# Kernel optimization log

Hardware: AMD Instinct MI355X
Metric: run time of the kernel (lower is better)

Reference implementation:

```python
import jax, jax.numpy as jnp
import numpy as np


def setup_inputs() -> dict:
    key = jax.random.key(0)
    k1, k2, k3, k4 = jax.random.split(key, 4)
    T, H, E, I = 4096, 1024, 8, 3584
    return {
        "hidden_states": jax.random.normal(k1, (T, H), dtype=jnp.float32),
        "gate_w": jax.random.normal(k2, (H, E), dtype=jnp.float32) * 0.02,
        "w1": jax.random.normal(k3, (E, H, I), dtype=jnp.float32) * 0.02,
        "w2": jax.random.normal(k4, (E, I, H), dtype=jnp.float32) * 0.02,
        "top_k": 2,
    }


def reference(hidden_states, gate_w, w1, w2, top_k):
    # Router: logits -> softmax -> top-k -> renormalize (Mixtral / vLLM fused_moe)
    router_logits = hidden_states @ gate_w                    # [T, E]
    probs = jax.nn.softmax(router_logits, axis=-1)
    top_vals, top_idx = jax.lax.top_k(probs, top_k)           # [T, K]
    top_vals = top_vals / jnp.sum(top_vals, axis=-1, keepdims=True)
    E = gate_w.shape[1]
    # Dense per-(token, expert) combine weights, zero for non-selected experts
    dense_w = jnp.sum(jax.nn.one_hot(top_idx, E, dtype=hidden_states.dtype)
                      * top_vals[..., None], axis=1)          # [T, E]
    # Expert MLP: silu(x @ w1[e]) @ w2[e], weighted by routing probs
    act = jax.nn.silu(jnp.einsum('th,ehi->tei', hidden_states, w1))  # [T, E, I]
    act = act * dense_w[:, :, None]
    out = jnp.einsum('tei,eih->th', act, w2)                  # [T, H]
    return out
```

## Files before the change

### kernel.cpp

```cpp
#include <hip/hip_runtime.h>
#include <hip/hip_bf16.h>

#define T_TOK 4096
#define H_DIM 1024
#define E_NUM 8
#define I_DIM 3584
#define NPAIR (T_TOK * 2)
#define MAX_RT 72

#define BM 128
#define BN 128
#define BK 64

typedef __attribute__((ext_vector_type(8))) short bf16x8;
typedef __attribute__((ext_vector_type(4))) float f32x4;
typedef __attribute__((ext_vector_type(8))) unsigned short ushort8_t;
typedef __attribute__((ext_vector_type(4))) unsigned short ushort4_t;

__device__ __forceinline__ unsigned short f2bf(float x) {
  unsigned int u = __float_as_uint(x);
  unsigned int r = (u + 0x7FFFu + ((u >> 16) & 1u)) >> 16;
  return (unsigned short)r;
}

__device__ __forceinline__ void gload16(const void* g, unsigned short* l) {
  __builtin_amdgcn_global_load_lds(
      (const __attribute__((address_space(1))) void*)g,
      (__attribute__((address_space(3))) void*)l, 16, 0, 0);
}

__global__ void transpose_cvt(const float* __restrict__ src,
                              unsigned short* __restrict__ dst, int R, int C) {
  __shared__ float tile[64][65];
  const int e = blockIdx.z;
  const int c0 = blockIdx.x * 64, r0 = blockIdx.y * 64;
  const float* s = src + (size_t)e * R * C;
  unsigned short* d = dst + (size_t)e * R * C;
  const int th = threadIdx.x;
  const int tr = th >> 4;
  const int tc4 = (th & 15) * 4;
#pragma unroll
  for (int it = 0; it < 4; ++it) {
    const int r = it * 16 + tr;
    float4 v = *reinterpret_cast<const float4*>(s + (size_t)(r0 + r) * C + c0 + tc4);
    tile[r][tc4] = v.x; tile[r][tc4 + 1] = v.y; tile[r][tc4 + 2] = v.z; tile[r][tc4 + 3] = v.w;
  }
  __syncthreads();
  const int wc = th >> 3;
  const int wr = (th & 7) * 8;
#pragma unroll
  for (int it = 0; it < 2; ++it) {
    const int c = it * 32 + wc;
    ushort8_t o;
#pragma unroll
    for (int j = 0; j < 8; ++j) o[j] = f2bf(tile[wr + j][c]);
    *reinterpret_cast<ushort8_t*>(d + (size_t)(c0 + c) * R + r0 + wr) = o;
  }
}

__global__ void router_kernel(const float* __restrict__ hs, const float* __restrict__ gw,
                              unsigned short* __restrict__ hsb,
                              int* __restrict__ eid, float* __restrict__ wgt,
                              int* __restrict__ counts) {
  __shared__ float s_gw[8192];
  __shared__ int s_cnt[E_NUM];
  const int th = threadIdx.x;
  for (int u = th; u < 2048; u += 256) {
    const f32x4 v = *reinterpret_cast<const f32x4*>(gw + u * 4);
    *reinterpret_cast<f32x4*>(&s_gw[(u ^ ((u >> 3) & 7)) * 4]) = v;
  }
  if (th < E_NUM) s_cnt[th] = 0;
  __syncthreads();

  const int l = th & 63, w = th >> 6;
#pragma unroll 1
  for (int tt = 0; tt < 4; ++tt) {
    const int t = blockIdx.x * 16 + w * 4 + tt;
    const float* hrow = hs + (size_t)t * H_DIM;
    unsigned short* brow = hsb + (size_t)t * H_DIM;
    float acc[E_NUM];
#pragma unroll
    for (int e = 0; e < E_NUM; ++e) acc[e] = 0.f;
#pragma unroll
    for (int i = 0; i < 4; ++i) {
      const int h0 = i * 256 + l * 4;
      const f32x4 x = *reinterpret_cast<const f32x4*>(hrow + h0);
      ushort4_t o = { f2bf(x[0]), f2bf(x[1]), f2bf(x[2]), f2bf(x[3]) };
      *reinterpret_cast<ushort4_t*>(brow + h0) = o;
#pragma unroll
      for (int j = 0; j < 4; ++j) {
        const int h = h0 + j;
        const int p0 = (h * 2) ^ ((h >> 2) & 7);
        const f32x4 g0 = *reinterpret_cast<const f32x4*>(&s_gw[p0 * 4]);
        const f32x4 g1 = *reinterpret_cast<const f32x4*>(&s_gw[(p0 ^ 1) * 4]);
        acc[0] += x[j] * g0[0]; acc[1] += x[j] * g0[1];
        acc[2] += x[j] * g0[2]; acc[3] += x[j] * g0[3];
        acc[4] += x[j] * g1[0]; acc[5] += x[j] * g1[1];
        acc[6] += x[j] * g1[2]; acc[7] += x[j] * g1[3];
      }
    }
#pragma unroll
    for (int e = 0; e < E_NUM; ++e) {
#pragma unroll
      for (int off = 1; off < 64; off <<= 1) acc[e] += __shfl_xor(acc[e], off);
    }
    if (l == 0) {
      int i1 = 0;
#pragma unroll
      for (int e = 1; e < E_NUM; ++e) if (acc[e] > acc[i1]) i1 = e;
      int i2 = (i1 == 0) ? 1 : 0;
#pragma unroll
      for (int e = 0; e < E_NUM; ++e) if (e != i1 && acc[e] > acc[i2]) i2 = e;
      const float e2 = __expf(acc[i2] - acc[i1]);
      const float inv = 1.f / (1.f + e2);
      eid[t * 2] = i1;     wgt[t * 2] = inv;
      eid[t * 2 + 1] = i2; wgt[t * 2 + 1] = e2 * inv;
      atomicAdd(&s_cnt[i1], 1);
      atomicAdd(&s_cnt[i2], 1);
    }
  }
  __syncthreads();
  if (th < E_NUM && s_cnt[th] > 0) atomicAdd(&counts[th], s_cnt[th]);
}

__global__ void scatter_kernel(const int* __restrict__ eid, const int* __restrict__ counts,
                               int* __restrict__ fill, int* __restrict__ rowmap) {
  __shared__ int hist[E_NUM], base[E_NUM];
  const int th = threadIdx.x;
  const int p = blockIdx.x * 256 + th;
  if (th < E_NUM) hist[th] = 0;
  __syncthreads();
  const int e = eid[p];
  const int rloc = atomicAdd(&hist[e], 1);
  __syncthreads();
  if (th < E_NUM) base[th] = (hist[th] > 0) ? atomicAdd(&fill[th], hist[th]) : 0;
  __syncthreads();
  int off = 0;
#pragma unroll
  for (int i = 0; i < E_NUM; ++i) off += (i < e) ? counts[i] : 0;
  rowmap[off + base[e] + rloc] = p;
}

template <int MODE, int NCT>
__launch_bounds__(256, 3)
__global__ void moe_gemm(const unsigned short* __restrict__ hsb,
                         const unsigned short* __restrict__ wt,
                         const unsigned short* __restrict__ act_in,
                         unsigned short* __restrict__ act_out,
                         float* __restrict__ out,
                         const int* __restrict__ counts,
                         const int* __restrict__ rowmap,
                         const float* __restrict__ wgt) {
  constexpr int KD = (MODE == 0) ? H_DIM : I_DIM;
  constexpr int NWG = MAX_RT * NCT;

  __shared__ unsigned short As[BM * BK];
  __shared__ unsigned short Bs[BN * BK];
  __shared__ int s_pair[BM];
  __shared__ float s_w[BM];

  const int bid = blockIdx.x;
  const int wgid = (bid & 7) * (NWG / 8) + (bid >> 3);
  const int rt = wgid / NCT;
  const int ct = wgid % NCT;

  int e = -1, loc_rt = 0, off_e = 0, cnt = 0;
  {
    int acc_t = 0, off = 0;
#pragma unroll
    for (int ee = 0; ee < E_NUM; ++ee) {
      const int c = counts[ee];
      const int nt = (c + BM - 1) >> 7;
      if (e < 0 && rt < acc_t + nt) { e = ee; loc_rt = rt - acc_t; off_e = off; cnt = c; }
      acc_t += nt; off += c;
    }
  }
  if (e < 0) return;

  const int cnt_local = min(BM, cnt - loc_rt * BM);
  const int r_base = off_e + loc_rt * BM;
  const int th = threadIdx.x;
  const int lane = th & 63, wid = th >> 6;

  if (MODE == 1 && th < BM) {
    int r = loc_rt * BM + th;
    if (r >= cnt) r = cnt - 1;
    const int p = rowmap[off_e + r];
    s_pair[th] = p;
    s_w[th] = wgt[p];
  }

  const int n0 = ct * BN;
  const unsigned short* wbase = wt + (size_t)e * ((size_t)I_DIM * H_DIM) + (size_t)n0 * KD;

  const int srow = lane >> 3;
  const int cg = (lane & 7) ^ srow;
  const char* aptr[4];
  const char* bptr[4];
#pragma unroll
  for (int i = 0; i < 4; ++i) {
    const int r = i * 32 + wid * 8 + srow;
    const int rr = (r < cnt_local) ? r : (cnt_local - 1);
    if (MODE == 0) {
      const int tok = rowmap[off_e + loc_rt * BM + rr] >> 1;
      aptr[i] = (const char*)(hsb + (size_t)tok * H_DIM) + cg * 16;
    } else {
      aptr[i] = (const char*)(act_in + (size_t)(r_base + rr) * I_DIM) + cg * 16;
    }
    bptr[i] = (const char*)(wbase + (size_t)r * KD) + cg * 16;
  }
  unsigned short* dstA[4];
  unsigned short* dstB[4];
#pragma unroll
  for (int i = 0; i < 4; ++i) {
    dstA[i] = &As[(i * 32 + wid * 8) * BK];
    dstB[i] = &Bs[(i * 32 + wid * 8) * BK];
  }

  f32x4 acc[4][4];
#pragma unroll
  for (int m = 0; m < 4; ++m)
#pragma unroll
    for (int n = 0; n < 4; ++n) acc[m][n] = (f32x4){0.f, 0.f, 0.f, 0.f};

  const int wm = (wid >> 1) * 64;
  const int wn = (wid & 1) * 64;
  const int fr = lane & 15;
  const int fq = lane >> 4;
  const int sxor = fr & 7;

  for (int k0 = 0; k0 < KD; k0 += BK) {
    const int kb = k0 * 2;
#pragma unroll
    for (int i = 0; i < 4; ++i) gload16(aptr[i] + kb, dstA[i]);
#pragma unroll
    for (int i = 0; i < 4; ++i) gload16(bptr[i] + kb, dstB[i]);
    __syncthreads();

#pragma unroll
    for (int kk = 0; kk < 2; ++kk) {
      bf16x8 af[4], bf[4];
#pragma unroll
      for (int m = 0; m < 4; ++m)
        af[m] = *reinterpret_cast<const bf16x8*>(
            &As[(wm + m * 16 + fr) * BK + ((kk * 4 + fq) ^ sxor) * 8]);
#pragma unroll
      for (int n = 0; n < 4; ++n)
        bf[n] = *reinterpret_cast<const bf16x8*>(
            &Bs[(wn + n * 16 + fr) * BK + ((kk * 4 + fq) ^ sxor) * 8]);
#pragma unroll
      for (int m = 0; m < 4; ++m)
#pragma unroll
        for (int n = 0; n < 4; ++n)
          acc[m][n] = __builtin_amdgcn_mfma_f32_16x16x32_bf16(af[m], bf[n], acc[m][n], 0, 0, 0);
    }
    __syncthreads();
  }

#pragma unroll
  for (int m = 0; m < 4; ++m) {
    const int row = wm + m * 16 + fq * 4;
#pragma unroll
    for (int n = 0; n < 4; ++n) {
      const int col = wn + n * 16 + fr;
#pragma unroll
      for (int r = 0; r < 4; ++r) {
        const int rw = row + r;
        if (rw < cnt_local) {
          const float x = acc[m][n][r];
          if (MODE == 0) {
            const float s = x / (1.f + __expf(-x));
            act_out[(size_t)(r_base + rw) * I_DIM + n0 + col] = f2bf(s);
          } else {
            const int p = s_pair[rw];
            const int tok = p >> 1;
            atomicAdd(out + (size_t)tok * H_DIM + n0 + col, x * s_w[rw]);
          }
        }
      }
    }
  }
}

extern "C" void kernel_launch(void* const* d_in, const int* in_sizes, int n_in,
                              void* d_out, int out_size, void* d_ws, size_t ws_size,
                              hipStream_t stream) {
  const float* hs = (const float*)d_in[0];
  const float* gw = (const float*)d_in[1];
  const float* w1 = (const float*)d_in[2];
  const float* w2 = (const float*)d_in[3];
  float* out = (float*)d_out;

  char* ws = (char*)d_ws;
  const size_t WMAT = (size_t)E_NUM * I_DIM * H_DIM * 2;
  unsigned short* w1t = (unsigned short*)ws;
  unsigned short* w2t = (unsigned short*)(ws + WMAT);
  unsigned short* act = (unsigned short*)(ws + 2 * WMAT);
  unsigned short* hsb = (unsigned short*)(ws + 3 * WMAT);
  char* small = ws + 3 * WMAT + (size_t)T_TOK * H_DIM * 2;
  int* eid = (int*)small;
  float* wgt = (float*)(small + NPAIR * 4);
  int* rowmap = (int*)(small + 2 * NPAIR * 4);
  int* counts = (int*)(small + 3 * NPAIR * 4);
  int* fill = counts + 8;

  hipMemsetAsync(d_out, 0, (size_t)T_TOK * H_DIM * sizeof(float), stream);
  hipMemsetAsync(counts, 0, 16 * sizeof(int), stream);

  transpose_cvt<<<dim3(I_DIM / 64, H_DIM / 64, E_NUM), 256, 0, stream>>>(w1, w1t, H_DIM, I_DIM);
  transpose_cvt<<<dim3(H_DIM / 64, I_DIM / 64, E_NUM), 256, 0, stream>>>(w2, w2t, I_DIM, H_DIM);

  router_kernel<<<T_TOK / 16, 256, 0, stream>>>(hs, gw, hsb, eid, wgt, counts);
  scatter_kernel<<<NPAIR / 256, 256, 0, stream>>>(eid, counts, fill, rowmap);

  moe_gemm<0, I_DIM / BN><<<MAX_RT * (I_DIM / BN), 256, 0, stream>>>(
      hsb, w1t, nullptr, act, nullptr, counts, rowmap, wgt);
  moe_gemm<1, H_DIM / BN><<<MAX_RT * (H_DIM / BN), 256, 0, stream>>>(
      hsb, w2t, act, nullptr, out, counts, rowmap, wgt);
}
```

Measured before the change: 286.4 us.

## Pipeline MoE GEMM with triple-buffered LDS ring, 256-wide tiles and split-K down-projection

Reworks the expert GEMM into a 512-thread workgroup with 128x256 tiles and a three-stage LDS ring buffer. Global-to-LDS loads for later K steps are issued while MFMAs run on the current stage, with explicit waitcnt, barriers and setprio. The second GEMM is split along K into four chunks that accumulate through the existing atomics, which restores parallelism after widening N. This raises LDS use and occupancy pressure and adds more atomic traffic on the output.

```diff
diff --git a/kernel.cpp b/kernel.cpp
--- a/kernel.cpp
+++ b/kernel.cpp
@@ -9,7 +9,7 @@
 #define MAX_RT 72
 
 #define BM 128
-#define BN 128
+#define BN 256
 #define BK 64
 
 typedef __attribute__((ext_vector_type(8))) short bf16x8;
@@ -141,8 +141,8 @@
   rowmap[off + base[e] + rloc] = p;
 }
 
-template <int MODE, int NCT>
-__launch_bounds__(256, 3)
+template <int MODE, int NCT, int KS, int KBLK>
+__launch_bounds__(512, 2)
 __global__ void moe_gemm(const unsigned short* __restrict__ hsb,
                          const unsigned short* __restrict__ wt,
                          const unsigned short* __restrict__ act_in,
@@ -151,18 +151,21 @@
                          const int* __restrict__ counts,
                          const int* __restrict__ rowmap,
                          const float* __restrict__ wgt) {
-  constexpr int KD = (MODE == 0) ? H_DIM : I_DIM;
-  constexpr int NWG = MAX_RT * NCT;
-
-  __shared__ unsigned short As[BM * BK];
-  __shared__ unsigned short Bs[BN * BK];
+  constexpr int KROW = (MODE == 0) ? H_DIM : I_DIM;
+  constexpr int NT = KBLK / BK;
+  constexpr int NWG = MAX_RT * NCT * KS;
+  constexpr int RING = 24576;
+
+  __shared__ unsigned short S[3 * RING];
   __shared__ int s_pair[BM];
   __shared__ float s_w[BM];
 
   const int bid = blockIdx.x;
   const int wgid = (bid & 7) * (NWG / 8) + (bid >> 3);
-  const int rt = wgid / NCT;
-  const int ct = wgid % NCT;
+  const int rt = wgid / (NCT * KS);
+  const int rem = wgid % (NCT * KS);
+  const int ct = rem % NCT;
+  const int kbase = (rem / NCT) * KBLK;
 
   int e = -1, loc_rt = 0, off_e = 0, cnt = 0;
   {
@@ -191,31 +194,47 @@
   }
 
   const int n0 = ct * BN;
-  const unsigned short* wbase = wt + (size_t)e * ((size_t)I_DIM * H_DIM) + (size_t)n0 * KD;
-
-  const int srow = lane >> 3;
-  const int cg = (lane & 7) ^ srow;
-  const char* aptr[4];
+  const unsigned short* wbase =
+      wt + (size_t)e * ((size_t)I_DIM * H_DIM) + (size_t)n0 * KROW + kbase;
+
+  const int srow8 = lane >> 3;
+  const int cg = (lane & 7) ^ srow8;
+  const char* aptr[2];
   const char* bptr[4];
 #pragma unroll
-  for (int i = 0; i < 4; ++i) {
-    const int r = i * 32 + wid * 8 + srow;
+  for (int i = 0; i < 2; ++i) {
+    const int r = i * 64 + wid * 8 + srow8;
     const int rr = (r < cnt_local) ? r : (cnt_local - 1);
     if (MODE == 0) {
       const int tok = rowmap[off_e + loc_rt * BM + rr] >> 1;
-      aptr[i] = (const char*)(hsb + (size_t)tok * H_DIM) + cg * 16;
+      aptr[i] = (const char*)(hsb + (size_t)tok * H_DIM + kbase) + cg * 16;
     } else {
-      aptr[i] = (const char*)(act_in + (size_t)(r_base + rr) * I_DIM) + cg * 16;
-    }
-    bptr[i] = (const char*)(wbase + (size_t)r * KD) + cg * 16;
-  }
-  unsigned short* dstA[4];
-  unsigned short* dstB[4];
-#pragma unroll
-  for (int i = 0; i < 4; ++i) {
-    dstA[i] = &As[(i * 32 + wid * 8) * BK];
-    dstB[i] = &Bs[(i * 32 + wid * 8) * BK];
-  }
+      aptr[i] = (const char*)(act_in + (size_t)(r_base + rr) * I_DIM + kbase) + cg * 16;
+    }
+  }
+#pragma unroll
+  for (int j = 0; j < 4; ++j) {
+    const int r = j * 64 + wid * 8 + srow8;
+    bptr[j] = (const char*)(wbase + (size_t)r * KROW) + cg * 16;
+  }
+
+#define STG_P0(rg, kb) do {                                     \
+    gload16(aptr[0] + (kb), &S[(rg) * RING + wid * 512]);       \
+    gload16(aptr[1] + (kb), &S[(rg) * RING + 4096 + wid * 512]);\
+    gload16(bptr[0] + (kb), &S[(rg) * RING + 8192 + wid * 512]);} while (0)
+#define STG_P1(rg, kb) do {                                     \
+    gload16(bptr[1] + (kb), &S[(rg) * RING + 12288 + wid * 512]);\
+    gload16(bptr[2] + (kb), &S[(rg) * RING + 16384 + wid * 512]);\
+    gload16(bptr[3] + (kb), &S[(rg) * RING + 20480 + wid * 512]);} while (0)
+
+  const int wm = (wid >> 2) * 64;
+  const int wn = (wid & 3) * 64;
+  const int fr = lane & 15, fq = lane >> 4;
+  const int sx = fr & 7;
+  const int ck0 = (fq ^ sx) * 8;
+  const int ck1 = ((4 + fq) ^ sx) * 8;
+  const int arow = (wm + fr) * 64;
+  const int brow = (wn + fr) * 64;
 
   f32x4 acc[4][4];
 #pragma unroll
@@ -223,58 +242,87 @@
 #pragma unroll
     for (int n = 0; n < 4; ++n) acc[m][n] = (f32x4){0.f, 0.f, 0.f, 0.f};
 
-  const int wm = (wid >> 1) * 64;
-  const int wn = (wid & 1) * 64;
-  const int fr = lane & 15;
-  const int fq = lane >> 4;
-  const int sxor = fr & 7;
-
-  for (int k0 = 0; k0 < KD; k0 += BK) {
-    const int kb = k0 * 2;
-#pragma unroll
-    for (int i = 0; i < 4; ++i) gload16(aptr[i] + kb, dstA[i]);
-#pragma unroll
-    for (int i = 0; i < 4; ++i) gload16(bptr[i] + kb, dstB[i]);
-    __syncthreads();
-
-#pragma unroll
-    for (int kk = 0; kk < 2; ++kk) {
-      bf16x8 af[4], bf[4];
+  STG_P0(0, 0); STG_P1(0, 0);
+  STG_P0(1, 128); STG_P1(1, 128);
+  asm volatile("s_waitcnt vmcnt(6)" ::: "memory");
+  __builtin_amdgcn_s_barrier();
+
+  int rd = 0, wr = 2;
+  for (int t = 0; t < NT; ++t) {
+    const unsigned short* Ab = &S[rd * RING];
+    const unsigned short* Bb = Ab + 8192;
+    const int kb2 = (t + 2) * 128;
+    const bool stg = (t + 2) < NT;
+    {
+      bf16x8 a0[4], b0[4];
 #pragma unroll
       for (int m = 0; m < 4; ++m)
-        af[m] = *reinterpret_cast<const bf16x8*>(
-            &As[(wm + m * 16 + fr) * BK + ((kk * 4 + fq) ^ sxor) * 8]);
+        a0[m] = *reinterpret_cast<const bf16x8*>(&Ab[arow + m * 1024 + ck0]);
 #pragma unroll
       for (int n = 0; n < 4; ++n)
-        bf[n] = *reinterpret_cast<const bf16x8*>(
-            &Bs[(wn + n * 16 + fr) * BK + ((kk * 4 + fq) ^ sxor) * 8]);
+        b0[n] = *reinterpret_cast<const bf16x8*>(&Bb[brow + n * 1024 + ck0]);
+      if (stg) STG_P0(wr, kb2);
+      __builtin_amdgcn_s_barrier();
+      asm volatile("s_waitcnt lgkmcnt(0)" ::: "memory");
+      __builtin_amdgcn_sched_barrier(0);
+      __builtin_amdgcn_s_setprio(1);
 #pragma unroll
       for (int m = 0; m < 4; ++m)
 #pragma unroll
         for (int n = 0; n < 4; ++n)
-          acc[m][n] = __builtin_amdgcn_mfma_f32_16x16x32_bf16(af[m], bf[n], acc[m][n], 0, 0, 0);
-    }
-    __syncthreads();
-  }
+          acc[m][n] = __builtin_amdgcn_mfma_f32_16x16x32_bf16(a0[m], b0[n], acc[m][n], 0, 0, 0);
+      __builtin_amdgcn_s_setprio(0);
+      __builtin_amdgcn_s_barrier();
+    }
+    {
+      bf16x8 a1[4], b1[4];
+#pragma unroll
+      for (int m = 0; m < 4; ++m)
+        a1[m] = *reinterpret_cast<const bf16x8*>(&Ab[arow + m * 1024 + ck1]);
+#pragma unroll
+      for (int n = 0; n < 4; ++n)
+        b1[n] = *reinterpret_cast<const bf16x8*>(&Bb[brow + n * 1024 + ck1]);
+      if (stg) STG_P1(wr, kb2);
+      __builtin_amdgcn_s_barrier();
+      asm volatile("s_waitcnt lgkmcnt(0)" ::: "memory");
+      __builtin_amdgcn_sched_barrier(0);
+      __builtin_amdgcn_s_setprio(1);
+#pragma unroll
+      for (int m = 0; m < 4; ++m)
+#pragma unroll
+        for (int n = 0; n < 4; ++n)
+          acc[m][n] = __builtin_amdgcn_mfma_f32_16x16x32_bf16(a1[m], b1[n], acc[m][n], 0, 0, 0);
+      __builtin_amdgcn_s_setprio(0);
+    }
+    if (t + 1 < NT) {
+      if (stg) asm volatile("s_waitcnt vmcnt(6)" ::: "memory");
+      else     asm volatile("s_waitcnt vmcnt(0)" ::: "memory");
+      __builtin_amdgcn_sched_barrier(0);
+      __builtin_amdgcn_s_barrier();
+    }
+    rd = (rd == 2) ? 0 : rd + 1;
+    wr = (wr == 2) ? 0 : wr + 1;
+  }
+#undef STG_P0
+#undef STG_P1
 
 #pragma unroll
   for (int m = 0; m < 4; ++m) {
     const int row = wm + m * 16 + fq * 4;
 #pragma unroll
     for (int n = 0; n < 4; ++n) {
-      const int col = wn + n * 16 + fr;
-#pragma unroll
-      for (int r = 0; r < 4; ++r) {
-        const int rw = row + r;
+      const int col = n0 + wn + n * 16 + fr;
+#pragma unroll
+      for (int r2 = 0; r2 < 4; ++r2) {
+        const int rw = row + r2;
         if (rw < cnt_local) {
-          const float x = acc[m][n][r];
+          const float x = acc[m][n][r2];
           if (MODE == 0) {
             const float s = x / (1.f + __expf(-x));
-            act_out[(size_t)(r_base + rw) * I_DIM + n0 + col] = f2bf(s);
+            act_out[(size_t)(r_base + rw) * I_DIM + col] = f2bf(s);
           } else {
-            const int p = s_pair[rw];
-            const int tok = p >> 1;
-            atomicAdd(out + (size_t)tok * H_DIM + n0 + col, x * s_w[rw]);
+            const int tok = s_pair[rw] >> 1;
+            atomicAdd(out + (size_t)tok * H_DIM + col, x * s_w[rw]);
           }
         }
       }
@@ -313,8 +361,8 @@
   router_kernel<<<T_TOK / 16, 256, 0, stream>>>(hs, gw, hsb, eid, wgt, counts);
   scatter_kernel<<<NPAIR / 256, 256, 0, stream>>>(eid, counts, fill, rowmap);
 
-  moe_gemm<0, I_DIM / BN><<<MAX_RT * (I_DIM / BN), 256, 0, stream>>>(
+  moe_gemm<0, 14, 1, 1024><<<MAX_RT * 14, 512, 0, stream>>>(
       hsb, w1t, nullptr, act, nullptr, counts, rowmap, wgt);
-  moe_gemm<1, H_DIM / BN><<<MAX_RT * (H_DIM / BN), 256, 0, stream>>>(
+  moe_gemm<1, 4, 4, 896><<<MAX_RT * 4 * 4, 512, 0, stream>>>(
       hsb, w2t, act, nullptr, out, counts, rowmap, wgt);
 }
```

Result: slower. 371.4 us (+29.7%).

## Double-buffer LDS tiles to overlap global loads with MFMA compute

Applied to the files above, without the earlier changes.

Converts the MoE GEMM main loop to a two-stage LDS ping-pong: the next K-tile is prefetched directly into the alternate buffer while the current tile's fragments are read and fed to MFMAs, with one barrier per iteration instead of two. It also hoists all fragment loads ahead of the MFMA block and raises wave priority during the math. Doubling LDS means occupancy drops from 3 to 2 blocks per CU (launch bounds changed accordingly), which trades latency hiding by occupancy for explicit software pipelining.

```diff
diff --git a/kernel.cpp b/kernel.cpp
--- a/kernel.cpp
+++ b/kernel.cpp
@@ -142,7 +142,7 @@
 }
 
 template <int MODE, int NCT>
-__launch_bounds__(256, 3)
+__launch_bounds__(256, 2)
 __global__ void moe_gemm(const unsigned short* __restrict__ hsb,
                          const unsigned short* __restrict__ wt,
                          const unsigned short* __restrict__ act_in,
@@ -152,10 +152,11 @@
                          const int* __restrict__ rowmap,
                          const float* __restrict__ wgt) {
   constexpr int KD = (MODE == 0) ? H_DIM : I_DIM;
+  constexpr int NT = KD / BK;
   constexpr int NWG = MAX_RT * NCT;
 
-  __shared__ unsigned short As[BM * BK];
-  __shared__ unsigned short Bs[BN * BK];
+  __shared__ unsigned short As[2][BM * BK];
+  __shared__ unsigned short Bs[2][BN * BK];
   __shared__ int s_pair[BM];
   __shared__ float s_w[BM];
 
@@ -209,13 +210,14 @@
     }
     bptr[i] = (const char*)(wbase + (size_t)r * KD) + cg * 16;
   }
-  unsigned short* dstA[4];
-  unsigned short* dstB[4];
-#pragma unroll
-  for (int i = 0; i < 4; ++i) {
-    dstA[i] = &As[(i * 32 + wid * 8) * BK];
-    dstB[i] = &Bs[(i * 32 + wid * 8) * BK];
-  }
+  const int dso = (wid * 8) * BK;
+
+#define STAGE(buf, kb) do {                                               \
+    _Pragma("unroll") for (int i = 0; i < 4; ++i)                         \
+        gload16(aptr[i] + (kb), &As[buf][dso + i * 32 * BK]);             \
+    _Pragma("unroll") for (int i = 0; i < 4; ++i)                         \
+        gload16(bptr[i] + (kb), &Bs[buf][dso + i * 32 * BK]);             \
+  } while (0)
 
   f32x4 acc[4][4];
 #pragma unroll
@@ -229,33 +231,49 @@
   const int fq = lane >> 4;
   const int sxor = fr & 7;
 
-  for (int k0 = 0; k0 < KD; k0 += BK) {
-    const int kb = k0 * 2;
-#pragma unroll
-    for (int i = 0; i < 4; ++i) gload16(aptr[i] + kb, dstA[i]);
-#pragma unroll
-    for (int i = 0; i < 4; ++i) gload16(bptr[i] + kb, dstB[i]);
-    __syncthreads();
-
-#pragma unroll
-    for (int kk = 0; kk < 2; ++kk) {
-      bf16x8 af[4], bf[4];
+  STAGE(0, 0);
+  asm volatile("s_waitcnt vmcnt(0)" ::: "memory");
+  __builtin_amdgcn_s_barrier();
+
+  int cur = 0;
+  for (int t = 0; t < NT; ++t) {
+    if (t + 1 < NT) STAGE(cur ^ 1, (size_t)(t + 1) * BK * 2);
+    __builtin_amdgcn_sched_barrier(0);
+
+    bf16x8 af[4][2], bfq[4][2];
+#pragma unroll
+    for (int m = 0; m < 4; ++m)
+#pragma unroll
+      for (int kk = 0; kk < 2; ++kk)
+        af[m][kk] = *reinterpret_cast<const bf16x8*>(
+            &As[cur][(wm + m * 16 + fr) * BK + ((kk * 4 + fq) ^ sxor) * 8]);
+#pragma unroll
+    for (int n = 0; n < 4; ++n)
+#pragma unroll
+      for (int kk = 0; kk < 2; ++kk)
+        bfq[n][kk] = *reinterpret_cast<const bf16x8*>(
+            &Bs[cur][(wn + n * 16 + fr) * BK + ((kk * 4 + fq) ^ sxor) * 8]);
+    asm volatile("s_waitcnt lgkmcnt(0)" ::: "memory");
+    __builtin_amdgcn_sched_barrier(0);
+
+    __builtin_amdgcn_s_setprio(1);
+#pragma unroll
+    for (int kk = 0; kk < 2; ++kk)
 #pragma unroll
       for (int m = 0; m < 4; ++m)
-        af[m] = *reinterpret_cast<const bf16x8*>(
-            &As[(wm + m * 16 + fr) * BK + ((kk * 4 + fq) ^ sxor) * 8]);
-#pragma unroll
-      for (int n = 0; n < 4; ++n)
-        bf[n] = *reinterpret_cast<const bf16x8*>(
-            &Bs[(wn + n * 16 + fr) * BK + ((kk * 4 + fq) ^ sxor) * 8]);
-#pragma unroll
-      for (int m = 0; m < 4; ++m)
 #pragma unroll
         for (int n = 0; n < 4; ++n)
-          acc[m][n] = __builtin_amdgcn_mfma_f32_16x16x32_bf16(af[m], bf[n], acc[m][n], 0, 0, 0);
-    }
-    __syncthreads();
-  }
+          acc[m][n] = __builtin_amdgcn_mfma_f32_16x16x32_bf16(af[m][kk], bfq[n][kk], acc[m][n], 0, 0, 0);
+    __builtin_amdgcn_s_setprio(0);
+
+    if (t + 1 < NT) {
+      asm volatile("s_waitcnt vmcnt(0)" ::: "memory");
+      __builtin_amdgcn_sched_barrier(0);
+      __builtin_amdgcn_s_barrier();
+    }
+    cur ^= 1;
+  }
+#undef STAGE
 
 #pragma unroll
   for (int m = 0; m < 4; ++m) {
```

New measurement: 350.3 us. 22.3% more time.

## Split-K the down-projection GEMM and remap up-projection tiles for L2 locality

Applied to the files above, without the earlier changes.

The second expert GEMM now splits its K dimension (I=3584) into two halves, doubling the workgroup count so the small N=1024 output gets more parallelism. Partial sums go into the pre-zeroed fp32 output, presumably through atomics. The first GEMM gets a blocked row/column tile mapping (groups of 9 row tiles by 4 column tiles) meant to improve L2 reuse of weights and activations. Launch bounds rise to 4 waves per SIMD, which tightens the register budget and risks spills, and split-K adds atomic traffic.

```diff
diff --git a/kernel.cpp b/kernel.cpp
--- a/kernel.cpp
+++ b/kernel.cpp
@@ -141,8 +141,8 @@
   rowmap[off + base[e] + rloc] = p;
 }
 
-template <int MODE, int NCT>
-__launch_bounds__(256, 3)
+template <int MODE, int NCT, int KS>
+__launch_bounds__(256, 4)
 __global__ void moe_gemm(const unsigned short* __restrict__ hsb,
                          const unsigned short* __restrict__ wt,
                          const unsigned short* __restrict__ act_in,
@@ -151,8 +151,10 @@
                          const int* __restrict__ counts,
                          const int* __restrict__ rowmap,
                          const float* __restrict__ wgt) {
-  constexpr int KD = (MODE == 0) ? H_DIM : I_DIM;
-  constexpr int NWG = MAX_RT * NCT;
+  constexpr int KROW = (MODE == 0) ? H_DIM : I_DIM;
+  constexpr int KD = KROW / KS;
+  constexpr int NT = KD / BK;
+  constexpr int NWG = MAX_RT * NCT * KS;
 
   __shared__ unsigned short As[BM * BK];
   __shared__ unsigned short Bs[BN * BK];
@@ -161,8 +163,20 @@
 
   const int bid = blockIdx.x;
   const int wgid = (bid & 7) * (NWG / 8) + (bid >> 3);
-  const int rt = wgid / NCT;
-  const int ct = wgid % NCT;
+  int rt, ct, kbase;
+  if (MODE == 0) {
+    const int l = wgid % 252;
+    const int cb = (wgid / 252) * 9;
+    const int q = l % 36;
+    rt = cb + q % 9;
+    ct = (l / 36) * 4 + q / 9;
+    kbase = 0;
+  } else {
+    rt = wgid / (NCT * KS);
+    const int col = wgid % (NCT * KS);
+    ct = col % NCT;
+    kbase = (col / NCT) * KD;
+  }
 
   int e = -1, loc_rt = 0, off_e = 0, cnt = 0;
   {
@@ -191,7 +205,8 @@
   }
 
   const int n0 = ct * BN;
-  const unsigned short* wbase = wt + (size_t)e * ((size_t)I_DIM * H_DIM) + (size_t)n0 * KD;
+  const unsigned short* wbase =
+      wt + (size_t)e * ((size_t)I_DIM * H_DIM) + (size_t)n0 * KROW + kbase;
 
   const int srow = lane >> 3;
   const int cg = (lane & 7) ^ srow;
@@ -205,9 +220,9 @@
       const int tok = rowmap[off_e + loc_rt * BM + rr] >> 1;
       aptr[i] = (const char*)(hsb + (size_t)tok * H_DIM) + cg * 16;
     } else {
-      aptr[i] = (const char*)(act_in + (size_t)(r_base + rr) * I_DIM) + cg * 16;
-    }
-    bptr[i] = (const char*)(wbase + (size_t)r * KD) + cg * 16;
+      aptr[i] = (const char*)(act_in + (size_t)(r_base + rr) * I_DIM + kbase) + cg * 16;
+    }
+    bptr[i] = (const char*)(wbase + (size_t)r * KROW) + cg * 16;
   }
   unsigned short* dstA[4];
   unsigned short* dstB[4];
@@ -313,8 +328,8 @@
   router_kernel<<<T_TOK / 16, 256, 0, stream>>>(hs, gw, hsb, eid, wgt, counts);
   scatter_kernel<<<NPAIR / 256, 256, 0, stream>>>(eid, counts, fill, rowmap);
 
-  moe_gemm<0, I_DIM / BN><<<MAX_RT * (I_DIM / BN), 256, 0, stream>>>(
+  moe_gemm<0, I_DIM / BN, 1><<<MAX_RT * (I_DIM / BN), 256, 0, stream>>>(
       hsb, w1t, nullptr, act, nullptr, counts, rowmap, wgt);
-  moe_gemm<1, H_DIM / BN><<<MAX_RT * (H_DIM / BN), 256, 0, stream>>>(
+  moe_gemm<1, H_DIM / BN, 2><<<MAX_RT * (H_DIM / BN) * 2, 256, 0, stream>>>(
       hsb, w2t, act, nullptr, out, counts, rowmap, wgt);
 }
```

Result: slower. 309.7 us (+8.1%).
